# Optimization experiments

Hardware: AMD Instinct MI355X
Metric: run time of the kernel (lower is better)

Reference implementation:

```python
import jax, jax.numpy as jnp
import numpy as np

B, L, M, H, DK, DV, S, DM = 8, 512, 512, 8, 128, 128, 512, 1024
W_REC = M + L  # recent window length (xl cache + current block)
INF = 1e30
EPS = 1e-6
TAU = DK ** 0.5


def _ln(x):
    mu = jnp.mean(x, axis=-1, keepdims=True)
    xc = x - mu
    return xc * jax.lax.rsqrt(jnp.mean(xc * xc, axis=-1, keepdims=True) + EPS)


def _rel_shift(x):
    # Transformer-XL relative shift, x: (b,h,l,w)
    b, h, l, w = x.shape
    x = jnp.pad(x, ((0, 0), (0, 0), (0, 0), (1, 0)))
    return x.reshape(b, h, w + 1, l)[:, :, 1:, :].reshape(b, h, l, w)


def setup_inputs() -> dict:
    key = jax.random.key(0)
    ks = jax.random.split(key, 16)
    inv = 1.0 / np.sqrt(DM)
    return {
        "input_features": jax.random.normal(ks[0], (B, L, DM), jnp.float32),
        "loss_mask": jnp.ones((B, L), jnp.float32),
        "xl_k_hat": jax.random.normal(ks[1], (B, H, M, DK), jnp.float32),
        "xl_v": jax.random.normal(ks[2], (B, H, M, DV), jnp.float32),
        "agg_upper": jax.random.normal(ks[3], (B, H, S, DV), jnp.float32),
        "agg_lower": jax.random.uniform(ks[4], (B, H, S), jnp.float32),
        "W_q": jax.random.normal(ks[5], (DM, H * DK), jnp.float32) * inv,
        "W_kvg": jax.random.normal(ks[6], (DM, H * DK + 2 * H * DV), jnp.float32) * inv,
        "W_res": jax.random.normal(ks[7], (H * DV, DM), jnp.float32) * inv,
        "x_u": jax.random.normal(ks[8], (H, DK), jnp.float32) * 0.02,
        "x_v": jax.random.normal(ks[9], (H, DK), jnp.float32) * 0.02,
        "xl_r": jax.random.normal(ks[10], (H, W_REC, DK), jnp.float32) * inv,
        "codebook": jax.random.normal(ks[11], (H, S, DK), jnp.float32),
        "doc_ids": jnp.zeros((B, L), jnp.int64),
        "xl_z": jax.random.randint(ks[12], (B, H, M), 0, S).astype(jnp.int64),
    }


def _forward(input_features, loss_mask, xl_k_hat, xl_v, agg_upper, agg_lower,
             W_q, W_kvg, W_res, x_u, x_v, xl_r, codebook, doc_ids, xl_z):
    # ---- projections ----
    x_t = _ln(input_features)                                  # (B,L,DM)
    q = (x_t @ W_q).reshape(B, L, H, DK).transpose(0, 2, 1, 3)  # (B,H,L,DK)
    kvg = x_t @ W_kvg
    k = kvg[..., : H * DK].reshape(B, L, H, DK).transpose(0, 2, 1, 3)
    v = kvg[..., H * DK: H * DK + H * DV].reshape(B, L, H, DV).transpose(0, 2, 1, 3)
    g = jax.nn.silu(kvg[..., H * DK + H * DV:])                # (B,L,H*DV)
    # per-head LN of q, k (q_ln / k_ln, gain=False, bias=False)
    q = _ln(q)
    k = _ln(k)

    # ---- VQ quantize keys: nearest codeword per head, straight-through ----
    d2 = (jnp.sum(k * k, -1)[..., None]
          - 2.0 * jnp.einsum("bhlk,hsk->bhls", k, codebook)
          + jnp.sum(codebook * codebook, -1)[None, :, None, :])  # (B,H,L,S)
    z = jnp.argmin(d2, axis=-1)                                  # (B,H,L)
    c_z = codebook[jnp.arange(H)[None, :, None], z]              # (B,H,L,DK)
    k_hat = k + jax.lax.stop_gradient(c_z - k)

    # ---- recent (xl cache + present block) ----
    recent_k_hat = jnp.concatenate([xl_k_hat, k_hat], axis=2)    # (B,H,W,DK)
    recent_v = jnp.concatenate([xl_v, v], axis=2)                # (B,H,W,DV)

    qu = q + x_u[None, :, None, :]
    qv = q + x_v[None, :, None, :]

    # ---- aggregated codeword-cache scores with log-count biases ----
    cache_scores = jnp.einsum("bhlk,hsk->bhls", qu, codebook) / TAU
    cache_bias = jnp.where(agg_lower > 0,
                           jnp.log(jnp.maximum(agg_lower, 1e-30)), -INF)
    cache_scores = cache_scores + cache_bias[:, :, None, :]      # (B,H,L,S)

    # ---- recent scores: content (ac) + relative position (bd) ----
    sc_ac = jnp.einsum("bhlk,bhwk->bhlw", qu, recent_k_hat) / TAU
    sc_bd = _rel_shift(jnp.einsum("bhlk,hwk->bhlw", qv, xl_r) / TAU)
    # causal mask: query i (block position) sees recent position j iff j <= i + M
    mask = (jnp.arange(W_REC)[None, :] <= (jnp.arange(L)[:, None] + M))
    recent_scores = jnp.where(mask[None, None], sc_ac + sc_bd, -INF)

    # ---- joint stable softmax over {codewords} U {recent positions} ----
    m = jax.lax.stop_gradient(
        jnp.maximum(jnp.max(cache_scores, -1), jnp.max(recent_scores, -1)))
    cache_a = jnp.exp(cache_scores - m[..., None])
    recent_a = jnp.exp(recent_scores - m[..., None])
    denom = jnp.sum(recent_a, -1) + jnp.sum(cache_a, -1)         # (B,H,L)
    inv_d = 1.0 / denom

    wv = (jnp.einsum("bhlw,bhwv->bhlv", recent_a * inv_d[..., None], recent_v)
          + jnp.einsum("bhls,bhsv->bhlv", cache_a * inv_d[..., None], agg_upper))
    wv = wv.transpose(0, 2, 1, 3).reshape(B, L, H * DV)

    # ---- gate + residual projection (dropout = identity at p=0) ----
    res = (wv * g) @ W_res                                       # (B,L,DM)
    return res


def reference(input_features, loss_mask, xl_k_hat, xl_v, agg_upper, agg_lower,
              W_q, W_kvg, W_res, x_u, x_v, xl_r, codebook, doc_ids, xl_z):
    return _forward(input_features, loss_mask, xl_k_hat, xl_v, agg_upper,
                    agg_lower, W_q, W_kvg, W_res, x_u, x_v, xl_r, codebook,
                    doc_ids, xl_z)
```

## Files before the change

### kernel.cpp

```cpp
#include <hip/hip_runtime.h>

#define INF30 1e30f
#define INV_TAU 0.08838834764831845f

typedef unsigned short ushort_t;
typedef __attribute__((ext_vector_type(8))) short bf16x8;
typedef __attribute__((ext_vector_type(4))) float f32x4;
typedef __attribute__((ext_vector_type(8))) unsigned short us8;

__device__ __forceinline__ float4 ld4(const float* p) { return *(const float4*)p; }

__device__ __forceinline__ unsigned short bf16_rne(float x) {
    unsigned int u = __float_as_uint(x);
    unsigned int r = u + 0x7fffu + ((u >> 16) & 1u);
    return (unsigned short)(r >> 16);
}
__device__ __forceinline__ float bf16_tof(unsigned short h) {
    return __uint_as_float(((unsigned int)h) << 16);
}
__device__ __forceinline__ bf16x8 ldb8(const ushort_t* p) { return *(const bf16x8*)p; }

#define MFMA16(a, b, c) __builtin_amdgcn_mfma_f32_16x16x32_bf16((a), (b), (c), 0, 0, 0)

__global__ __launch_bounds__(256) void ln_dm_kernel(const float* __restrict__ x, float* __restrict__ y) {
    size_t row = blockIdx.x;
    const float4* xr = (const float4*)(x + row * 1024);
    float4 v = xr[threadIdx.x];
    float s  = v.x + v.y + v.z + v.w;
    float ss = v.x*v.x + v.y*v.y + v.z*v.z + v.w*v.w;
#pragma unroll
    for (int off = 32; off > 0; off >>= 1) {
        s  += __shfl_down(s, off);
        ss += __shfl_down(ss, off);
    }
    __shared__ float rs[4], rss[4];
    int wv = threadIdx.x >> 6, ln = threadIdx.x & 63;
    if (ln == 0) { rs[wv] = s; rss[wv] = ss; }
    __syncthreads();
    s  = rs[0] + rs[1] + rs[2] + rs[3];
    ss = rss[0] + rss[1] + rss[2] + rss[3];
    float mu  = s * (1.0f/1024.0f);
    float var = ss * (1.0f/1024.0f) - mu*mu;
    float r = rsqrtf(var + 1e-6f);
    float4 o;
    o.x = (v.x - mu) * r; o.y = (v.y - mu) * r; o.z = (v.z - mu) * r; o.w = (v.w - mu) * r;
    ((float4*)(y + row * 1024))[threadIdx.x] = o;
}

__global__ __launch_bounds__(256) void gemm_kernel(const float* __restrict__ A, const float* __restrict__ W,
                                                   int N, int mode,
                                                   float* __restrict__ o0, float* __restrict__ o1,
                                                   float* __restrict__ o2) {
    __shared__ float As[16][64];
    __shared__ float Bs[16][64];
    int t = threadIdx.x;
    int col0 = blockIdx.x << 6;
    int row0 = blockIdx.y << 6;
    int tx = t & 15, ty = t >> 4;
    int arow = t >> 2, akq = t & 3;
    int bkr = t >> 4, bcq = t & 15;
    const float* Ap = A + (size_t)(row0 + arow) * 1024 + akq * 4;
    const float* Wp = W + (size_t)bkr * N + col0 + bcq * 4;
    float acc[4][4];
#pragma unroll
    for (int i = 0; i < 4; ++i)
#pragma unroll
        for (int j = 0; j < 4; ++j) acc[i][j] = 0.0f;

    for (int kt = 0; kt < 64; ++kt) {
        float4 a4 = ld4(Ap + kt * 16);
        float4 b4 = ld4(Wp + (size_t)kt * 16 * N);
        __syncthreads();
        As[akq*4+0][arow] = a4.x;
        As[akq*4+1][arow] = a4.y;
        As[akq*4+2][arow] = a4.z;
        As[akq*4+3][arow] = a4.w;
        *(float4*)&Bs[bkr][bcq*4] = b4;
        __syncthreads();
#pragma unroll
        for (int kk = 0; kk < 16; ++kk) {
            float4 av = *(float4*)&As[kk][ty*4];
            float4 bv = *(float4*)&Bs[kk][tx*4];
            acc[0][0] += av.x*bv.x; acc[0][1] += av.x*bv.y; acc[0][2] += av.x*bv.z; acc[0][3] += av.x*bv.w;
            acc[1][0] += av.y*bv.x; acc[1][1] += av.y*bv.y; acc[1][2] += av.y*bv.z; acc[1][3] += av.y*bv.w;
            acc[2][0] += av.z*bv.x; acc[2][1] += av.z*bv.y; acc[2][2] += av.z*bv.z; acc[2][3] += av.z*bv.w;
            acc[3][0] += av.w*bv.x; acc[3][1] += av.w*bv.y; acc[3][2] += av.w*bv.z; acc[3][3] += av.w*bv.w;
        }
    }

#pragma unroll
    for (int i = 0; i < 4; ++i) {
        int rr = row0 + ty*4 + i;
        int b = rr >> 9, l = rr & 511;
#pragma unroll
        for (int j = 0; j < 4; ++j) {
            int cc = col0 + tx*4 + j;
            float vv = acc[i][j];
            if (mode == 0) {
                o0[((size_t)((b<<3) + (cc>>7)) * 512 + l) * 128 + (cc & 127)] = vv;
            } else if (mode == 1) {
                if (cc < 1024) {
                    o0[((size_t)((b<<3) + (cc>>7)) * 512 + l) * 128 + (cc & 127)] = vv;
                } else if (cc < 2048) {
                    int c2 = cc - 1024;
                    o1[((size_t)((b<<3) + (c2>>7)) * 512 + l) * 128 + (c2 & 127)] = vv;
                } else {
                    o2[(size_t)rr * 1024 + (cc - 2048)] = vv / (1.0f + __expf(-vv));
                }
            } else {
                o0[(size_t)rr * 1024 + cc] = vv;
            }
        }
    }
}

__global__ __launch_bounds__(256) void wtsplit_kernel(const float* __restrict__ W, int Ntot, int c0,
                                                      ushort_t* __restrict__ th, ushort_t* __restrict__ tl) {
    __shared__ float T[64][68];
    int n0 = blockIdx.x << 6, k0 = blockIdx.y << 6, t = threadIdx.x;
    for (int i = t; i < 1024; i += 256) {
        int kk = i >> 4, nn4 = (i & 15) << 2;
        *(float4*)&T[kk][nn4] = ld4(W + (size_t)(k0 + kk) * Ntot + c0 + n0 + nn4);
    }
    __syncthreads();
    for (int i = t; i < 512; i += 256) {
        int nn = i >> 3, kc = (i & 7) << 3;
        us8 h8, l8;
#pragma unroll
        for (int j = 0; j < 8; ++j) {
            float x = T[kc + j][nn];
            unsigned short hh = bf16_rne(x);
            h8[j] = hh; l8[j] = bf16_rne(x - bf16_tof(hh));
        }
        size_t off = (size_t)(n0 + nn) * 1024 + k0 + kc;
        *(us8*)(th + off) = h8;
        *(us8*)(tl + off) = l8;
    }
}

#define GSTRIDE 40
__global__ __launch_bounds__(256) void gemm_bf16_kernel(
        const ushort_t* __restrict__ Ah, const ushort_t* __restrict__ Al,
        const ushort_t* __restrict__ Bth, const ushort_t* __restrict__ Btl,
        int mode, float* __restrict__ o0, float* __restrict__ o1) {
    __shared__ ushort_t LA[2][128 * GSTRIDE];
    __shared__ ushort_t LB[2][128 * GSTRIDE];
    int t = threadIdx.x;
    int col0 = blockIdx.x << 7, row0 = blockIdx.y << 7;
    int wvid = t >> 6, ln = t & 63;
    int lcol = ln & 15, quad = ln >> 4;
    int qm = wvid >> 1, qn = wvid & 1;

    f32x4 C[4][4];
#pragma unroll
    for (int i = 0; i < 4; ++i)
#pragma unroll
        for (int j = 0; j < 4; ++j) C[i][j] = (f32x4){0.f, 0.f, 0.f, 0.f};

    for (int k0 = 0; k0 < 1024; k0 += 32) {
        us8 ra[2][2], rb[2][2];
#pragma unroll
        for (int v = 0; v < 2; ++v) {
            int cid = t + 256 * v;
            int row = cid >> 2, ch = cid & 3;
            size_t ga = (size_t)(row0 + row) * 1024 + k0 + ch * 8;
            size_t gb = (size_t)(col0 + row) * 1024 + k0 + ch * 8;
            ra[v][0] = *(const us8*)(Ah + ga);
            ra[v][1] = *(const us8*)(Al + ga);
            rb[v][0] = *(const us8*)(Bth + gb);
            rb[v][1] = *(const us8*)(Btl + gb);
        }
        __syncthreads();
#pragma unroll
        for (int v = 0; v < 2; ++v) {
            int cid = t + 256 * v;
            int row = cid >> 2, ch = cid & 3;
            *(us8*)&LA[0][row * GSTRIDE + ch * 8] = ra[v][0];
            *(us8*)&LA[1][row * GSTRIDE + ch * 8] = ra[v][1];
            *(us8*)&LB[0][row * GSTRIDE + ch * 8] = rb[v][0];
            *(us8*)&LB[1][row * GSTRIDE + ch * 8] = rb[v][1];
        }
        __syncthreads();
        bf16x8 afh[4], afl[4], bfh[4], bfl[4];
#pragma unroll
        for (int i = 0; i < 4; ++i) {
            int r = qm * 64 + i * 16 + lcol;
            afh[i] = *(const bf16x8*)&LA[0][r * GSTRIDE + quad * 8];
            afl[i] = *(const bf16x8*)&LA[1][r * GSTRIDE + quad * 8];
            int c = qn * 64 + i * 16 + lcol;
            bfh[i] = *(const bf16x8*)&LB[0][c * GSTRIDE + quad * 8];
            bfl[i] = *(const bf16x8*)&LB[1][c * GSTRIDE + quad * 8];
        }
#pragma unroll
        for (int i = 0; i < 4; ++i)
#pragma unroll
            for (int j = 0; j < 4; ++j) {
                C[i][j] = MFMA16(afh[i], bfh[j], C[i][j]);
                C[i][j] = MFMA16(afl[i], bfh[j], C[i][j]);
                C[i][j] = MFMA16(afh[i], bfl[j], C[i][j]);
            }
    }

#pragma unroll
    for (int i = 0; i < 4; ++i) {
#pragma unroll
        for (int r = 0; r < 4; ++r) {
            int rr = row0 + qm * 64 + 16 * i + quad * 4 + r;
            int b = rr >> 9, l = rr & 511;
#pragma unroll
            for (int j = 0; j < 4; ++j) {
                int cc = col0 + qn * 64 + 16 * j + lcol;
                float vv = C[i][j][r];
                if (mode == 0) {
                    o0[((size_t)((b<<3) + (cc>>7)) * 512 + l) * 128 + (cc & 127)] = vv;
                } else if (mode == 1) {
                    if (cc < 1024) o0[((size_t)((b<<3) + (cc>>7)) * 512 + l) * 128 + (cc & 127)] = vv;
                    else o1[(size_t)rr * 1024 + (cc - 1024)] = vv / (1.0f + __expf(-vv));
                } else {
                    o0[(size_t)rr * 1024 + cc] = vv;
                }
            }
        }
    }
}

__global__ __launch_bounds__(256) void ln128_kernel(float* __restrict__ qb, float* __restrict__ kb) {
    int wv = threadIdx.x >> 6, ln = threadIdx.x & 63;
    int gw = (blockIdx.x << 2) + wv;
    float* base = (gw < 32768) ? qb : kb;
    int row = gw & 32767;
    float2 x = *(float2*)(base + (size_t)row * 128 + (ln << 1));
    float s  = x.x + x.y;
    float ss = x.x*x.x + x.y*x.y;
#pragma unroll
    for (int m = 32; m > 0; m >>= 1) { s += __shfl_xor(s, m); ss += __shfl_xor(ss, m); }
    float mu  = s * (1.0f/128.0f);
    float var = ss * (1.0f/128.0f) - mu*mu;
    float r = rsqrtf(var + 1e-6f);
    x.x = (x.x - mu) * r; x.y = (x.y - mu) * r;
    *(float2*)(base + (size_t)row * 128 + (ln << 1)) = x;
}

__global__ __launch_bounds__(256) void cbt_kernel(const float* __restrict__ cb, float* __restrict__ cT) {
    int idx = blockIdx.x * 256 + threadIdx.x;
    int h = idx >> 16, s = (idx >> 7) & 511, d = idx & 127;
    cT[((size_t)((h << 7) + d)) * 512 + s] = cb[idx];
}

__global__ __launch_bounds__(256) void cnorm_kernel(const float* __restrict__ cb, float* __restrict__ cn) {
    int wv = threadIdx.x >> 6, ln = threadIdx.x & 63;
    int row = (blockIdx.x << 2) + wv;
    float2 x = *(const float2*)(cb + (size_t)row * 128 + (ln << 1));
    float ss = x.x*x.x + x.y*x.y;
#pragma unroll
    for (int m = 32; m > 0; m >>= 1) ss += __shfl_xor(ss, m);
    if (ln == 0) cn[row] = ss;
}

__global__ __launch_bounds__(256) void vq_kernel(float* __restrict__ kb, const float* __restrict__ cT,
                                                 const float* __restrict__ cn, const float* __restrict__ cb) {
    __shared__ float sK[4][4][128];
    int wv = threadIdx.x >> 6, ln = threadIdx.x & 63;
    int gw = (blockIdx.x << 2) + wv;
    int bh = gw >> 7;
    int l4 = (gw & 127) << 2;
    int h = bh & 7;
    size_t r0 = ((size_t)bh << 9) + l4;
#pragma unroll
    for (int i = 0; i < 4; ++i) {
        float2 kx = *(const float2*)(kb + (r0 + i) * 128 + (ln << 1));
        sK[wv][i][(ln<<1)]   = kx.x;
        sK[wv][i][(ln<<1)+1] = kx.y;
    }
    __syncthreads();
    const float* ct = cT + ((size_t)h << 7) * 512;
    int s0 = ln << 3;
    float dt[4][8];
#pragma unroll
    for (int i = 0; i < 4; ++i)
#pragma unroll
        for (int j = 0; j < 8; ++j) dt[i][j] = 0.0f;

    for (int dc = 0; dc < 4; ++dc) {
        float ch[4][8];
#pragma unroll
        for (int i = 0; i < 4; ++i)
#pragma unroll
            for (int j = 0; j < 8; ++j) ch[i][j] = 0.0f;
#pragma unroll 4
        for (int d = dc * 32; d < dc * 32 + 32; ++d) {
            float4 c0 = ld4(ct + (size_t)d * 512 + s0);
            float4 c1 = ld4(ct + (size_t)d * 512 + s0 + 4);
#pragma unroll
            for (int i = 0; i < 4; ++i) {
                float kd = sK[wv][i][d];
                ch[i][0] += kd * c0.x; ch[i][1] += kd * c0.y; ch[i][2] += kd * c0.z; ch[i][3] += kd * c0.w;
                ch[i][4] += kd * c1.x; ch[i][5] += kd * c1.y; ch[i][6] += kd * c1.z; ch[i][7] += kd * c1.w;
            }
        }
#pragma unroll
        for (int i = 0; i < 4; ++i)
#pragma unroll
            for (int j = 0; j < 8; ++j) dt[i][j] += ch[i][j];
    }
    const float* cnh = cn + (h << 9);
#pragma unroll
    for (int i = 0; i < 4; ++i) {
        float bestv = cnh[s0] - 2.0f * dt[i][0];
        int bestz = s0;
#pragma unroll
        for (int j = 1; j < 8; ++j) {
            float scv = cnh[s0 + j] - 2.0f * dt[i][j];
            if (scv < bestv) { bestv = scv; bestz = s0 + j; }
        }
#pragma unroll
        for (int m = 32; m > 0; m >>= 1) {
            float ov = __shfl_xor(bestv, m);
            int   oz = __shfl_xor(bestz, m);
            if (ov < bestv || (ov == bestv && oz < bestz)) { bestv = ov; bestz = oz; }
        }
        float2 cz = *(const float2*)(cb + ((size_t)(h << 9) + bestz) * 128 + (ln << 1));
        *(float2*)(kb + (r0 + i) * 128 + (ln << 1)) = cz;
    }
}

__global__ __launch_bounds__(256) void split_q_kernel(const float* __restrict__ q,
        const float* __restrict__ xu, const float* __restrict__ xv,
        ushort_t* __restrict__ quh, ushort_t* __restrict__ qul,
        ushort_t* __restrict__ qvh) {
    int idx = blockIdx.x * 256 + threadIdx.x;
    int d = idx & 127;
    int h = (idx >> 16) & 7;
    float qv = q[idx];
    float a = qv + xu[(h << 7) + d];
    unsigned short ah = bf16_rne(a);
    quh[idx] = ah; qul[idx] = bf16_rne(a - bf16_tof(ah));
    float b = qv + xv[(h << 7) + d];
    qvh[idx] = bf16_rne(b);
}

__global__ __launch_bounds__(256) void split_plain_kernel(const float* __restrict__ src,
        ushort_t* __restrict__ hi, ushort_t* __restrict__ lo) {
    int idx = blockIdx.x * 256 + threadIdx.x;
    float x = src[idx];
    unsigned short h = bf16_rne(x);
    hi[idx] = h; lo[idx] = bf16_rne(x - bf16_tof(h));
}

__global__ __launch_bounds__(256) void cvt_hi_kernel(const float* __restrict__ src,
        ushort_t* __restrict__ hi) {
    int idx = blockIdx.x * 256 + threadIdx.x;
    hi[idx] = bf16_rne(src[idx]);
}

__global__ __launch_bounds__(256) void split_koff_kernel(const float* __restrict__ src,
        ushort_t* __restrict__ hi, ushort_t* __restrict__ lo, int rowoff) {
    int idx = blockIdx.x * 256 + threadIdx.x;
    int bh = idx >> 16, rem = idx & 65535;
    size_t dst = ((size_t)bh << 17) + ((size_t)rowoff << 7) + rem;
    float x = src[idx];
    unsigned short h = bf16_rne(x);
    hi[dst] = h; lo[dst] = bf16_rne(x - bf16_tof(h));
}

__global__ __launch_bounds__(256) void vtsplit_kernel(const float* __restrict__ srcA,
        const float* __restrict__ srcB, ushort_t* __restrict__ hi, ushort_t* __restrict__ lo, int NK) {
    __shared__ float T[64][132];
    int bh = blockIdx.x, kt = blockIdx.y, t = threadIdx.x;
    for (int i = t; i < 2048; i += 256) {
        int r = i >> 5, c4 = (i & 31) << 2;
        int key = (kt << 6) + r;
        const float* s = (key < 512) ? (srcA + ((size_t)bh * 512 + key) * 128 + c4)
                                     : (srcB + ((size_t)bh * 512 + (key - 512)) * 128 + c4);
        *(float4*)&T[r][c4] = ld4(s);
    }
    __syncthreads();
    for (int i = t; i < 1024; i += 256) {
        int vc = i >> 3, kk = (i & 7) << 3;
        us8 h8, l8;
#pragma unroll
        for (int j = 0; j < 8; ++j) {
            float x = T[kk + j][vc];
            unsigned short hh = bf16_rne(x);
            h8[j] = hh; l8[j] = bf16_rne(x - bf16_tof(hh));
        }
        size_t off = ((size_t)bh * 128 + vc) * NK + (kt << 6) + kk;
        *(us8*)(hi + off) = h8;
        *(us8*)(lo + off) = l8;
    }
}

__global__ __launch_bounds__(256) void cbias_kernel(const float* __restrict__ al, float* __restrict__ cb) {
    int idx = blockIdx.x * 256 + threadIdx.x;
    float v = al[idx];
    cb[idx] = (v > 0.0f) ? __logf(fmaxf(v, 1e-30f)) : -INF30;
}

#define PSTR 40
__global__ __launch_bounds__(256) void attn4_kernel(
        const ushort_t* __restrict__ Qu_hi, const ushort_t* __restrict__ Qu_lo,
        const ushort_t* __restrict__ Qv_hi,
        const ushort_t* __restrict__ K_hi,  const ushort_t* __restrict__ K_lo,
        const ushort_t* __restrict__ C_hi,  const ushort_t* __restrict__ C_lo,
        const ushort_t* __restrict__ Vt_hi, const ushort_t* __restrict__ Vt_lo,
        const ushort_t* __restrict__ At_hi, const ushort_t* __restrict__ At_lo,
        const ushort_t* __restrict__ R_hi,
        const float* __restrict__ cbias, const float* __restrict__ gbuf,
        float* __restrict__ wvg) {
    __shared__ __align__(16) ushort_t Phs[4][16 * PSTR];
    __shared__ __align__(16) ushort_t Pls[4][16 * PSTR];
    __shared__ float Oc[2][16 * 132];
    __shared__ float mc[2][16], lc[2][16];

    int t = threadIdx.x;
    int wvid = t >> 6, ln = t & 63;
    int col = ln & 15, quad = ln >> 4;
    int bh = blockIdx.x >> 4;
    int tg = blockIdx.x & 15;
    int tile = (wvid & 2) ? (tg + 16) : tg;
    int q = wvid & 1;
    int l0w = tile << 4;
    int h = bh & 7;
    int b = bh >> 3;

    ushort_t* Ph = Phs[wvid];
    ushort_t* Pl = Pls[wvid];

    bf16x8 quh[4], qul[4], qvh[4];
    {
        size_t base = ((size_t)bh * 512 + l0w + col) * 128 + quad * 8;
#pragma unroll
        for (int s = 0; s < 4; ++s) {
            quh[s] = ldb8(Qu_hi + base + 32 * s);
            qul[s] = ldb8(Qu_lo + base + 32 * s);
            qvh[s] = ldb8(Qv_hi + base + 32 * s);
        }
    }

    f32x4 O[8];
#pragma unroll
    for (int u = 0; u < 8; ++u) O[u] = (f32x4){0.f, 0.f, 0.f, 0.f};
    float mrun[4], lrun[4];
#pragma unroll
    for (int r = 0; r < 4; ++r) { mrun[r] = -INF30; lrun[r] = 0.0f; }

    int nt2 = (l0w + 47) >> 5;
    int T = 32 + nt2;
    int half = (T + 1) >> 1;
    int ti0 = q ? half : 0;
    int ti1 = q ? T : half;

    for (int ti = ti0; ti < ti1; ++ti) {
        int seg, w0;
        if (ti < 16)      { seg = 0; w0 = ti << 5; }
        else if (ti < 32) { seg = 1; w0 = (ti - 16) << 5; }
        else              { seg = 2; w0 = (ti - 32) << 5; }

        f32x4 Gacc[3];
        if (seg != 1) {
            int jt0 = ((seg == 0) ? w0 : (512 + w0)) + 496 - l0w;
#pragma unroll
            for (int u = 0; u < 3; ++u) {
                int j = jt0 + 16 * u + col;
                j = (j > 1023) ? 1023 : j;
                const ushort_t* rp = R_hi + ((size_t)(h << 10) + j) * 128 + quad * 8;
                f32x4 acc = (f32x4){0.f, 0.f, 0.f, 0.f};
#pragma unroll
                for (int s = 0; s < 4; ++s) acc = MFMA16(qvh[s], ldb8(rp + 32 * s), acc);
                Gacc[u] = acc;
            }
        }

        const ushort_t *khb, *klb;
        if (seg == 0)      { khb = K_hi + ((size_t)bh * 1024 + w0) * 128;
                             klb = K_lo + ((size_t)bh * 1024 + w0) * 128; }
        else if (seg == 1) { khb = C_hi + ((size_t)(h << 9) + w0) * 128;
                             klb = C_lo + ((size_t)(h << 9) + w0) * 128; }
        else               { khb = K_hi + ((size_t)bh * 1024 + 512 + w0) * 128;
                             klb = K_lo + ((size_t)bh * 1024 + 512 + w0) * 128; }
        f32x4 S[2];
#pragma unroll
        for (int t2 = 0; t2 < 2; ++t2) {
            const ushort_t* kph = khb + (size_t)(16 * t2 + col) * 128 + quad * 8;
            const ushort_t* kpl = klb + (size_t)(16 * t2 + col) * 128 + quad * 8;
            bf16x8 bhf[4], blf[4];
#pragma unroll
            for (int s = 0; s < 4; ++s) { bhf[s] = ldb8(kph + 32 * s); blf[s] = ldb8(kpl + 32 * s); }
            f32x4 acc = (f32x4){0.f, 0.f, 0.f, 0.f};
#pragma unroll
            for (int s = 0; s < 4; ++s) {
                acc = MFMA16(quh[s], bhf[s], acc);
                acc = MFMA16(qul[s], bhf[s], acc);
                acc = MFMA16(quh[s], blf[s], acc);
            }
            S[t2] = acc;
        }

        float bias0 = 0.f, bias1 = 0.f;
        if (seg == 1) {
            bias0 = cbias[(size_t)(bh << 9) + w0 + col];
            bias1 = cbias[(size_t)(bh << 9) + w0 + 16 + col];
        }
#pragma unroll
        for (int t2 = 0; t2 < 2; ++t2) {
#pragma unroll
            for (int r = 0; r < 4; ++r) {
                int row = 4 * quad + r;
                float sv = S[t2][r];
                if (seg != 1) {
                    int d = col + 15 - row;
                    int src = quad * 16 + (d & 15);
                    float g0 = __shfl(Gacc[t2][r], src);
                    float g1 = __shfl(Gacc[t2 + 1][r], src);
                    float gv = (d >= 16) ? g1 : g0;
                    sv = (sv + gv) * INV_TAU;
                    if (seg == 2 && (w0 + 16 * t2 + col > l0w + row)) sv = -INF30;
                } else {
                    sv = sv * INV_TAU + ((t2 == 0) ? bias0 : bias1);
                }
                S[t2][r] = sv;
            }
        }

#pragma unroll
        for (int r = 0; r < 4; ++r) {
            float mv = fmaxf(S[0][r], S[1][r]);
#pragma unroll
            for (int m = 8; m > 0; m >>= 1) mv = fmaxf(mv, __shfl_xor(mv, m));
            float mnew = fmaxf(mrun[r], mv);
            float alpha = __expf(mrun[r] - mnew);
            mrun[r] = mnew;
            float p0 = __expf(S[0][r] - mnew);
            float p1 = __expf(S[1][r] - mnew);
            float ps = p0 + p1;
#pragma unroll
            for (int m = 8; m > 0; m >>= 1) ps += __shfl_xor(ps, m);
            lrun[r] = lrun[r] * alpha + ps;
#pragma unroll
            for (int u = 0; u < 8; ++u) O[u][r] *= alpha;
            int row = 4 * quad + r;
            unsigned short h0 = bf16_rne(p0);
            Ph[row * PSTR + col] = h0;
            Pl[row * PSTR + col] = bf16_rne(p0 - bf16_tof(h0));
            unsigned short h1 = bf16_rne(p1);
            Ph[row * PSTR + 16 + col] = h1;
            Pl[row * PSTR + 16 + col] = bf16_rne(p1 - bf16_tof(h1));
        }

        bf16x8 pah = *(const bf16x8*)&Ph[col * PSTR + quad * 8];
        bf16x8 pal = *(const bf16x8*)&Pl[col * PSTR + quad * 8];

        const ushort_t *vh, *vl;
        size_t vstr;
        int wbase;
        if (seg == 0)      { vh = Vt_hi + ((size_t)bh << 17); vl = Vt_lo + ((size_t)bh << 17); vstr = 1024; wbase = w0; }
        else if (seg == 1) { vh = At_hi + ((size_t)bh << 16); vl = At_lo + ((size_t)bh << 16); vstr = 512;  wbase = w0; }
        else               { vh = Vt_hi + ((size_t)bh << 17); vl = Vt_lo + ((size_t)bh << 17); vstr = 1024; wbase = 512 + w0; }
#pragma unroll
        for (int u = 0; u < 8; ++u) {
            int vcol = 16 * u + col;
            bf16x8 vbh = ldb8(vh + (size_t)vcol * vstr + wbase + quad * 8);
            bf16x8 vbl = ldb8(vl + (size_t)vcol * vstr + wbase + quad * 8);
            O[u] = MFMA16(pah, vbh, O[u]);
            O[u] = MFMA16(pal, vbh, O[u]);
            O[u] = MFMA16(pah, vbl, O[u]);
        }
    }

    if (q) {
        int i = wvid >> 1;
#pragma unroll
        for (int u = 0; u < 8; ++u)
#pragma unroll
            for (int r = 0; r < 4; ++r)
                Oc[i][(quad * 4 + r) * 132 + 16 * u + col] = O[u][r];
        if (col == 0) {
#pragma unroll
            for (int r = 0; r < 4; ++r) {
                mc[i][quad * 4 + r] = mrun[r];
                lc[i][quad * 4 + r] = lrun[r];
            }
        }
    }
    __syncthreads();
    if (!q) {
        int i = wvid >> 1;
#pragma unroll
        for (int r = 0; r < 4; ++r) {
            int row = quad * 4 + r;
            float m1 = mc[i][row], l1 = lc[i][row];
            float mm = fmaxf(mrun[r], m1);
            float a0 = __expf(mrun[r] - mm);
            float a1 = __expf(m1 - mm);
            float linv = 1.0f / (lrun[r] * a0 + l1 * a1);
#pragma unroll
            for (int u = 0; u < 8; ++u) {
                size_t gi = ((size_t)b * 512 + l0w + row) * 1024 + (h << 7) + 16 * u + col;
                float val = (O[u][r] * a0 + Oc[i][row * 132 + 16 * u + col] * a1) * linv;
                wvg[gi] = val * gbuf[gi];
            }
        }
    }
}

extern "C" void kernel_launch(void* const* d_in, const int* in_sizes, int n_in,
                              void* d_out, int out_size, void* d_ws, size_t ws_size,
                              hipStream_t stream) {
    const float* x_in  = (const float*)d_in[0];
    const float* xl_k  = (const float*)d_in[2];
    const float* xl_v  = (const float*)d_in[3];
    const float* agg_u = (const float*)d_in[4];
    const float* agg_l = (const float*)d_in[5];
    const float* W_q   = (const float*)d_in[6];
    const float* W_kvg = (const float*)d_in[7];
    const float* W_res = (const float*)d_in[8];
    const float* x_u   = (const float*)d_in[9];
    const float* x_v   = (const float*)d_in[10];
    const float* xl_r  = (const float*)d_in[11];
    const float* cbk   = (const float*)d_in[12];
    float* out = (float*)d_out;
    char* wb = (char*)d_ws;

    float*  x_t   = (float*)(wb);
    float*  qbuf  = (float*)(wb + 16777216ul);
    float*  kbuf  = (float*)(wb + 33554432ul);
    float*  vbuf  = (float*)(wb + 50331648ul);
    float*  gbuf  = (float*)(wb + 67108864ul);
    float*  wvg   = (float*)(wb + 83886080ul);
    float*  cT    = (float*)(wb + 100663296ul);
    float*  cnm   = (float*)(wb + 102760448ul);
    ushort_t* Qu_hi = (ushort_t*)(wb + 102776832ul);
    ushort_t* Qu_lo = (ushort_t*)(wb + 111165440ul);
    ushort_t* Qv_hi = (ushort_t*)(wb + 119554048ul);
    ushort_t* K_lo  = (ushort_t*)(wb + 136331264ul);
    ushort_t* R_hi  = (ushort_t*)(wb + 153108480ul);
    float*  cbias   = (float*)(wb + 157302784ul);

    ushort_t* K_hi  = (ushort_t*)x_t;
    ushort_t* Vt_hi = (ushort_t*)kbuf;
    ushort_t* Vt_lo = (ushort_t*)qbuf;
    ushort_t* At_hi = (ushort_t*)vbuf;
    ushort_t* At_lo = (ushort_t*)(wb + 50331648ul + 8388608ul);
    ushort_t* C_hi  = (ushort_t*)cT;
    ushort_t* C_lo  = (ushort_t*)(wb + 100663296ul + 1048576ul);

    ushort_t* Ah      = (ushort_t*)wvg;
    ushort_t* Al      = (ushort_t*)(wb + 83886080ul + 8388608ul);
    ushort_t* Wtq_hi  = (ushort_t*)Qu_hi;
    ushort_t* Wtq_lo  = (ushort_t*)(wb + 102776832ul + 2097152ul);
    ushort_t* Wtvg_hi = (ushort_t*)Qu_lo;
    ushort_t* Wtvg_lo = (ushort_t*)(wb + 111165440ul + 4194304ul);
    ushort_t* Wtres_hi = (ushort_t*)Qv_hi;
    ushort_t* Wtres_lo = (ushort_t*)(wb + 119554048ul + 2097152ul);
    ushort_t* Awh     = (ushort_t*)x_t;
    ushort_t* Awl     = (ushort_t*)(wb + 8388608ul);

    ln_dm_kernel<<<4096, 256, 0, stream>>>(x_in, x_t);
    split_plain_kernel<<<16384, 256, 0, stream>>>(x_t, Ah, Al);
    wtsplit_kernel<<<dim3(16, 16), 256, 0, stream>>>(W_q, 1024, 0, Wtq_hi, Wtq_lo);
    wtsplit_kernel<<<dim3(32, 16), 256, 0, stream>>>(W_kvg, 3072, 1024, Wtvg_hi, Wtvg_lo);
    gemm_bf16_kernel<<<dim3(8, 32), 256, 0, stream>>>(Ah, Al, Wtq_hi, Wtq_lo, 0, qbuf, nullptr);
    gemm_bf16_kernel<<<dim3(16, 32), 256, 0, stream>>>(Ah, Al, Wtvg_hi, Wtvg_lo, 1, vbuf, gbuf);
    gemm_kernel<<<dim3(16, 64), 256, 0, stream>>>(x_t, W_kvg, 3072, 0, kbuf, nullptr, nullptr);
    ln128_kernel<<<16384, 256, 0, stream>>>(qbuf, kbuf);
    cbt_kernel<<<2048, 256, 0, stream>>>(cbk, cT);
    cnorm_kernel<<<1024, 256, 0, stream>>>(cbk, cnm);
    vq_kernel<<<2048, 256, 0, stream>>>(kbuf, cT, cnm, cbk);
    split_q_kernel<<<16384, 256, 0, stream>>>(qbuf, x_u, x_v, Qu_hi, Qu_lo, Qv_hi);
    split_koff_kernel<<<16384, 256, 0, stream>>>(xl_k, K_hi, K_lo, 0);
    split_koff_kernel<<<16384, 256, 0, stream>>>(kbuf, K_hi, K_lo, 512);
    split_plain_kernel<<<2048, 256, 0, stream>>>(cbk, C_hi, C_lo);
    cvt_hi_kernel<<<4096, 256, 0, stream>>>(xl_r, R_hi);
    vtsplit_kernel<<<dim3(64, 16), 256, 0, stream>>>(xl_v, vbuf, Vt_hi, Vt_lo, 1024);
    vtsplit_kernel<<<dim3(64, 8), 256, 0, stream>>>(agg_u, agg_u, At_hi, At_lo, 512);
    cbias_kernel<<<128, 256, 0, stream>>>(agg_l, cbias);
    attn4_kernel<<<1024, 256, 0, stream>>>(Qu_hi, Qu_lo, Qv_hi, K_hi, K_lo, C_hi, C_lo,
                                           Vt_hi, Vt_lo, At_hi, At_lo, R_hi,
                                           cbias, gbuf, wvg);
    split_plain_kernel<<<16384, 256, 0, stream>>>(wvg, Awh, Awl);
    wtsplit_kernel<<<dim3(16, 16), 256, 0, stream>>>(W_res, 1024, 0, Wtres_hi, Wtres_lo);
    gemm_bf16_kernel<<<dim3(8, 32), 256, 0, stream>>>(Awh, Awl, Wtres_hi, Wtres_lo, 2, out, nullptr);
}
```

Baseline: 1.035 ms.

## Pair mirrored query tiles per wave to share K/V loads and balance causal work

Each wave now processes two 16-row query tiles, one near the start and one near the end of the sequence (pairj and 31-pairj). Each K/V/codebook load is reused by both tiles, which halves global key/value traffic per query, and the pairing evens out the causal triangle work across waves. The grid halves to 512 blocks, blocks are remapped so the same bh lands on one XCD for L2 locality, and the kernel gets launch_bounds(256,2). The split point between the two cooperating waves is fixed at step 20. Costs: higher register pressure from doubled accumulators and Q fragments, more LDS, and Qv is reloaded from global each step instead of being held in registers.

```diff
diff --git a/kernel.cpp b/kernel.cpp
--- a/kernel.cpp
+++ b/kernel.cpp
@@ -397,7 +397,7 @@
 }
 
 #define PSTR 40
-__global__ __launch_bounds__(256) void attn4_kernel(
+__global__ __launch_bounds__(256, 2) void attn5_kernel(
         const ushort_t* __restrict__ Qu_hi, const ushort_t* __restrict__ Qu_lo,
         const ushort_t* __restrict__ Qv_hi,
         const ushort_t* __restrict__ K_hi,  const ushort_t* __restrict__ K_lo,
@@ -407,67 +407,83 @@
         const ushort_t* __restrict__ R_hi,
         const float* __restrict__ cbias, const float* __restrict__ gbuf,
         float* __restrict__ wvg) {
-    __shared__ __align__(16) ushort_t Phs[4][16 * PSTR];
-    __shared__ __align__(16) ushort_t Pls[4][16 * PSTR];
-    __shared__ float Oc[2][16 * 132];
-    __shared__ float mc[2][16], lc[2][16];
+    __shared__ __align__(16) ushort_t Phs[4][2][16 * PSTR];
+    __shared__ __align__(16) ushort_t Pls[4][2][16 * PSTR];
+    __shared__ float Oc[4][16 * 132];
+    __shared__ float mc[4][16], lc[4][16];
 
     int t = threadIdx.x;
     int wvid = t >> 6, ln = t & 63;
     int col = ln & 15, quad = ln >> 4;
-    int bh = blockIdx.x >> 4;
-    int tg = blockIdx.x & 15;
-    int tile = (wvid & 2) ? (tg + 16) : tg;
-    int q = wvid & 1;
-    int l0w = tile << 4;
-    int h = bh & 7;
-    int b = bh >> 3;
-
-    ushort_t* Ph = Phs[wvid];
-    ushort_t* Pl = Pls[wvid];
-
-    bf16x8 quh[4], qul[4], qvh[4];
-    {
-        size_t base = ((size_t)bh * 512 + l0w + col) * 128 + quad * 8;
+    int blk = blockIdx.x;
+    int xcd = blk & 7, idx = blk >> 3;
+    int bh = ((idx >> 3) << 3) + xcd;
+    int sub = idx & 7;
+    int wp = wvid >> 1, q = wvid & 1;
+    int pairj = (sub << 1) + wp;
+    int l0[2];
+    l0[0] = pairj << 4;
+    l0[1] = (31 - pairj) << 4;
+    int h = bh & 7, b = bh >> 3;
+
+    bf16x8 quh[2][4], qul[2][4];
+#pragma unroll
+    for (int tt = 0; tt < 2; ++tt) {
+        size_t base = ((size_t)bh * 512 + l0[tt] + col) * 128 + quad * 8;
 #pragma unroll
         for (int s = 0; s < 4; ++s) {
-            quh[s] = ldb8(Qu_hi + base + 32 * s);
-            qul[s] = ldb8(Qu_lo + base + 32 * s);
-            qvh[s] = ldb8(Qv_hi + base + 32 * s);
-        }
-    }
-
-    f32x4 O[8];
-#pragma unroll
-    for (int u = 0; u < 8; ++u) O[u] = (f32x4){0.f, 0.f, 0.f, 0.f};
-    float mrun[4], lrun[4];
-#pragma unroll
-    for (int r = 0; r < 4; ++r) { mrun[r] = -INF30; lrun[r] = 0.0f; }
-
-    int nt2 = (l0w + 47) >> 5;
-    int T = 32 + nt2;
-    int half = (T + 1) >> 1;
-    int ti0 = q ? half : 0;
-    int ti1 = q ? T : half;
+            quh[tt][s] = ldb8(Qu_hi + base + 32 * s);
+            qul[tt][s] = ldb8(Qu_lo + base + 32 * s);
+        }
+    }
+
+    f32x4 O[2][8];
+#pragma unroll
+    for (int tt = 0; tt < 2; ++tt)
+#pragma unroll
+        for (int u = 0; u < 8; ++u) O[tt][u] = (f32x4){0.f, 0.f, 0.f, 0.f};
+    float mrun[2][4], lrun[2][4];
+#pragma unroll
+    for (int tt = 0; tt < 2; ++tt)
+#pragma unroll
+        for (int r = 0; r < 4; ++r) { mrun[tt][r] = -INF30; lrun[tt][r] = 0.0f; }
+
+    int nt2A = (l0[0] + 47) >> 5;
+    int nt2B = (l0[1] + 47) >> 5;
+    int Tt = 32 + nt2B;
+    int ti0 = q ? 20 : 0;
+    int ti1 = q ? Tt : 20;
 
     for (int ti = ti0; ti < ti1; ++ti) {
         int seg, w0;
         if (ti < 16)      { seg = 0; w0 = ti << 5; }
         else if (ti < 32) { seg = 1; w0 = (ti - 16) << 5; }
         else              { seg = 2; w0 = (ti - 32) << 5; }
-
-        f32x4 Gacc[3];
+        bool actA = (seg != 2) || ((ti - 32) < nt2A);
+
+        f32x4 Gacc[2][3];
         if (seg != 1) {
-            int jt0 = ((seg == 0) ? w0 : (512 + w0)) + 496 - l0w;
-#pragma unroll
-            for (int u = 0; u < 3; ++u) {
-                int j = jt0 + 16 * u + col;
-                j = (j > 1023) ? 1023 : j;
-                const ushort_t* rp = R_hi + ((size_t)(h << 10) + j) * 128 + quad * 8;
-                f32x4 acc = (f32x4){0.f, 0.f, 0.f, 0.f};
-#pragma unroll
-                for (int s = 0; s < 4; ++s) acc = MFMA16(qvh[s], ldb8(rp + 32 * s), acc);
-                Gacc[u] = acc;
+#pragma unroll
+            for (int tt = 0; tt < 2; ++tt) {
+                if (tt == 0 && !actA) continue;
+                size_t qb_ = ((size_t)bh * 512 + l0[tt] + col) * 128 + quad * 8;
+                bf16x8 qv0 = ldb8(Qv_hi + qb_);
+                bf16x8 qv1 = ldb8(Qv_hi + qb_ + 32);
+                bf16x8 qv2 = ldb8(Qv_hi + qb_ + 64);
+                bf16x8 qv3 = ldb8(Qv_hi + qb_ + 96);
+                int jt0 = ((seg == 0) ? w0 : (512 + w0)) + 496 - l0[tt];
+#pragma unroll
+                for (int u = 0; u < 3; ++u) {
+                    int j = jt0 + 16 * u + col;
+                    j = (j > 1023) ? 1023 : j;
+                    const ushort_t* rp = R_hi + ((size_t)(h << 10) + j) * 128 + quad * 8;
+                    f32x4 acc = (f32x4){0.f, 0.f, 0.f, 0.f};
+                    acc = MFMA16(qv0, ldb8(rp), acc);
+                    acc = MFMA16(qv1, ldb8(rp + 32), acc);
+                    acc = MFMA16(qv2, ldb8(rp + 64), acc);
+                    acc = MFMA16(qv3, ldb8(rp + 96), acc);
+                    Gacc[tt][u] = acc;
+                }
             }
         }
 
@@ -478,7 +494,7 @@
                              klb = C_lo + ((size_t)(h << 9) + w0) * 128; }
         else               { khb = K_hi + ((size_t)bh * 1024 + 512 + w0) * 128;
                              klb = K_lo + ((size_t)bh * 1024 + 512 + w0) * 128; }
-        f32x4 S[2];
+        f32x4 S[2][2];
 #pragma unroll
         for (int t2 = 0; t2 < 2; ++t2) {
             const ushort_t* kph = khb + (size_t)(16 * t2 + col) * 128 + quad * 8;
@@ -486,14 +502,18 @@
             bf16x8 bhf[4], blf[4];
 #pragma unroll
             for (int s = 0; s < 4; ++s) { bhf[s] = ldb8(kph + 32 * s); blf[s] = ldb8(kpl + 32 * s); }
-            f32x4 acc = (f32x4){0.f, 0.f, 0.f, 0.f};
-#pragma unroll
-            for (int s = 0; s < 4; ++s) {
-                acc = MFMA16(quh[s], bhf[s], acc);
-                acc = MFMA16(qul[s], bhf[s], acc);
-                acc = MFMA16(quh[s], blf[s], acc);
-            }
-            S[t2] = acc;
+#pragma unroll
+            for (int tt = 0; tt < 2; ++tt) {
+                if (tt == 0 && !actA) continue;
+                f32x4 acc = (f32x4){0.f, 0.f, 0.f, 0.f};
+#pragma unroll
+                for (int s = 0; s < 4; ++s) {
+                    acc = MFMA16(quh[tt][s], bhf[s], acc);
+                    acc = MFMA16(qul[tt][s], bhf[s], acc);
+                    acc = MFMA16(quh[tt][s], blf[s], acc);
+                }
+                S[tt][t2] = acc;
+            }
         }
 
         float bias0 = 0.f, bias1 = 0.f;
@@ -501,54 +521,59 @@
             bias0 = cbias[(size_t)(bh << 9) + w0 + col];
             bias1 = cbias[(size_t)(bh << 9) + w0 + 16 + col];
         }
-#pragma unroll
-        for (int t2 = 0; t2 < 2; ++t2) {
+        bf16x8 pah[2], pal[2];
+#pragma unroll
+        for (int tt = 0; tt < 2; ++tt) {
+            if (tt == 0 && !actA) continue;
+            ushort_t* Ph = Phs[wvid][tt];
+            ushort_t* Pl = Pls[wvid][tt];
+#pragma unroll
+            for (int t2 = 0; t2 < 2; ++t2) {
+#pragma unroll
+                for (int r = 0; r < 4; ++r) {
+                    int row = 4 * quad + r;
+                    float sv = S[tt][t2][r];
+                    if (seg != 1) {
+                        int d = col + 15 - row;
+                        int src = quad * 16 + (d & 15);
+                        float g0 = __shfl(Gacc[tt][t2][r], src);
+                        float g1 = __shfl(Gacc[tt][t2 + 1][r], src);
+                        float gv = (d >= 16) ? g1 : g0;
+                        sv = (sv + gv) * INV_TAU;
+                        if (seg == 2 && (w0 + 16 * t2 + col > l0[tt] + row)) sv = -INF30;
+                    } else {
+                        sv = sv * INV_TAU + ((t2 == 0) ? bias0 : bias1);
+                    }
+                    S[tt][t2][r] = sv;
+                }
+            }
 #pragma unroll
             for (int r = 0; r < 4; ++r) {
+                float mv = fmaxf(S[tt][0][r], S[tt][1][r]);
+#pragma unroll
+                for (int m = 8; m > 0; m >>= 1) mv = fmaxf(mv, __shfl_xor(mv, m));
+                float mnew = fmaxf(mrun[tt][r], mv);
+                float alpha = __expf(mrun[tt][r] - mnew);
+                mrun[tt][r] = mnew;
+                float p0 = __expf(S[tt][0][r] - mnew);
+                float p1 = __expf(S[tt][1][r] - mnew);
+                float ps = p0 + p1;
+#pragma unroll
+                for (int m = 8; m > 0; m >>= 1) ps += __shfl_xor(ps, m);
+                lrun[tt][r] = lrun[tt][r] * alpha + ps;
+#pragma unroll
+                for (int u = 0; u < 8; ++u) O[tt][u][r] *= alpha;
                 int row = 4 * quad + r;
-                float sv = S[t2][r];
-                if (seg != 1) {
-                    int d = col + 15 - row;
-                    int src = quad * 16 + (d & 15);
-                    float g0 = __shfl(Gacc[t2][r], src);
-                    float g1 = __shfl(Gacc[t2 + 1][r], src);
-                    float gv = (d >= 16) ? g1 : g0;
-                    sv = (sv + gv) * INV_TAU;
-                    if (seg == 2 && (w0 + 16 * t2 + col > l0w + row)) sv = -INF30;
-                } else {
-                    sv = sv * INV_TAU + ((t2 == 0) ? bias0 : bias1);
-                }
-                S[t2][r] = sv;
-            }
-        }
-
-#pragma unroll
-        for (int r = 0; r < 4; ++r) {
-            float mv = fmaxf(S[0][r], S[1][r]);
-#pragma unroll
-            for (int m = 8; m > 0; m >>= 1) mv = fmaxf(mv, __shfl_xor(mv, m));
-            float mnew = fmaxf(mrun[r], mv);
-            float alpha = __expf(mrun[r] - mnew);
-            mrun[r] = mnew;
-            float p0 = __expf(S[0][r] - mnew);
-            float p1 = __expf(S[1][r] - mnew);
-            float ps = p0 + p1;
-#pragma unroll
-            for (int m = 8; m > 0; m >>= 1) ps += __shfl_xor(ps, m);
-            lrun[r] = lrun[r] * alpha + ps;
-#pragma unroll
-            for (int u = 0; u < 8; ++u) O[u][r] *= alpha;
-            int row = 4 * quad + r;
-            unsigned short h0 = bf16_rne(p0);
-            Ph[row * PSTR + col] = h0;
-            Pl[row * PSTR + col] = bf16_rne(p0 - bf16_tof(h0));
-            unsigned short h1 = bf16_rne(p1);
-            Ph[row * PSTR + 16 + col] = h1;
-            Pl[row * PSTR + 16 + col] = bf16_rne(p1 - bf16_tof(h1));
-        }
-
-        bf16x8 pah = *(const bf16x8*)&Ph[col * PSTR + quad * 8];
-        bf16x8 pal = *(const bf16x8*)&Pl[col * PSTR + quad * 8];
+                unsigned short h0 = bf16_rne(p0);
+                Ph[row * PSTR + col] = h0;
+                Pl[row * PSTR + col] = bf16_rne(p0 - bf16_tof(h0));
+                unsigned short h1 = bf16_rne(p1);
+                Ph[row * PSTR + 16 + col] = h1;
+                Pl[row * PSTR + 16 + col] = bf16_rne(p1 - bf16_tof(h1));
+            }
+            pah[tt] = *(const bf16x8*)&Ph[col * PSTR + quad * 8];
+            pal[tt] = *(const bf16x8*)&Pl[col * PSTR + quad * 8];
+        }
 
         const ushort_t *vh, *vl;
         size_t vstr;
@@ -561,43 +586,53 @@
             int vcol = 16 * u + col;
             bf16x8 vbh = ldb8(vh + (size_t)vcol * vstr + wbase + quad * 8);
             bf16x8 vbl = ldb8(vl + (size_t)vcol * vstr + wbase + quad * 8);
-            O[u] = MFMA16(pah, vbh, O[u]);
-            O[u] = MFMA16(pal, vbh, O[u]);
-            O[u] = MFMA16(pah, vbl, O[u]);
+#pragma unroll
+            for (int tt = 0; tt < 2; ++tt) {
+                if (tt == 0 && !actA) continue;
+                O[tt][u] = MFMA16(pah[tt], vbh, O[tt][u]);
+                O[tt][u] = MFMA16(pal[tt], vbh, O[tt][u]);
+                O[tt][u] = MFMA16(pah[tt], vbl, O[tt][u]);
+            }
         }
     }
 
     if (q) {
-        int i = wvid >> 1;
-#pragma unroll
-        for (int u = 0; u < 8; ++u)
-#pragma unroll
-            for (int r = 0; r < 4; ++r)
-                Oc[i][(quad * 4 + r) * 132 + 16 * u + col] = O[u][r];
-        if (col == 0) {
-#pragma unroll
-            for (int r = 0; r < 4; ++r) {
-                mc[i][quad * 4 + r] = mrun[r];
-                lc[i][quad * 4 + r] = lrun[r];
+#pragma unroll
+        for (int tt = 0; tt < 2; ++tt) {
+            int sid = wp * 2 + tt;
+#pragma unroll
+            for (int u = 0; u < 8; ++u)
+#pragma unroll
+                for (int r = 0; r < 4; ++r)
+                    Oc[sid][(quad * 4 + r) * 132 + 16 * u + col] = O[tt][u][r];
+            if (col == 0) {
+#pragma unroll
+                for (int r = 0; r < 4; ++r) {
+                    mc[sid][quad * 4 + r] = mrun[tt][r];
+                    lc[sid][quad * 4 + r] = lrun[tt][r];
+                }
             }
         }
     }
     __syncthreads();
     if (!q) {
-        int i = wvid >> 1;
-#pragma unroll
-        for (int r = 0; r < 4; ++r) {
-            int row = quad * 4 + r;
-            float m1 = mc[i][row], l1 = lc[i][row];
-            float mm = fmaxf(mrun[r], m1);
-            float a0 = __expf(mrun[r] - mm);
-            float a1 = __expf(m1 - mm);
-            float linv = 1.0f / (lrun[r] * a0 + l1 * a1);
-#pragma unroll
-            for (int u = 0; u < 8; ++u) {
-                size_t gi = ((size_t)b * 512 + l0w + row) * 1024 + (h << 7) + 16 * u + col;
-                float val = (O[u][r] * a0 + Oc[i][row * 132 + 16 * u + col] * a1) * linv;
-                wvg[gi] = val * gbuf[gi];
+#pragma unroll
+        for (int tt = 0; tt < 2; ++tt) {
+            int sid = wp * 2 + tt;
+#pragma unroll
+            for (int r = 0; r < 4; ++r) {
+                int row = quad * 4 + r;
+                float m1 = mc[sid][row], l1 = lc[sid][row];
+                float mm = fmaxf(mrun[tt][r], m1);
+                float a0 = __expf(mrun[tt][r] - mm);
+                float a1 = __expf(m1 - mm);
+                float linv = 1.0f / (lrun[tt][r] * a0 + l1 * a1);
+#pragma unroll
+                for (int u = 0; u < 8; ++u) {
+                    size_t gi = ((size_t)b * 512 + l0[tt] + row) * 1024 + (h << 7) + 16 * u + col;
+                    float val = (O[tt][u][r] * a0 + Oc[sid][row * 132 + 16 * u + col] * a1) * linv;
+                    wvg[gi] = val * gbuf[gi];
+                }
             }
         }
     }
@@ -674,9 +709,9 @@
     vtsplit_kernel<<<dim3(64, 16), 256, 0, stream>>>(xl_v, vbuf, Vt_hi, Vt_lo, 1024);
     vtsplit_kernel<<<dim3(64, 8), 256, 0, stream>>>(agg_u, agg_u, At_hi, At_lo, 512);
     cbias_kernel<<<128, 256, 0, stream>>>(agg_l, cbias);
-    attn4_kernel<<<1024, 256, 0, stream>>>(Qu_hi, Qu_lo, Qv_hi, K_hi, K_lo, C_hi, C_lo,
-                                           Vt_hi, Vt_lo, At_hi, At_lo, R_hi,
-                                           cbias, gbuf, wvg);
+    attn5_kernel<<<512, 256, 0, stream>>>(Qu_hi, Qu_lo, Qv_hi, K_hi, K_lo, C_hi, C_lo,
+                                          Vt_hi, Vt_lo, At_hi, At_lo, R_hi,
+                                          cbias, gbuf, wvg);
     split_plain_kernel<<<16384, 256, 0, stream>>>(wvg, Awh, Awl);
     wtsplit_kernel<<<dim3(16, 16), 256, 0, stream>>>(W_res, 1024, 0, Wtres_hi, Wtres_lo);
     gemm_bf16_kernel<<<dim3(8, 32), 256, 0, stream>>>(Awh, Awl, Wtres_hi, Wtres_lo, 2, out, nullptr);
```

After: 930.8 us. -10.1%, faster.
